# Kernel tuning notes

Hardware: AMD Instinct MI355X
Metric: run time of the kernel (lower is better)

The kernel has to match this reference:

```python
import jax, jax.numpy as jnp
import numpy as np

N_NODES = 4096
EDGE_PROB = 0.01


def setup_inputs() -> dict:
    key = jax.random.key(0)
    kx, ka, kw = jax.random.split(key, 3)
    x = jax.random.normal(kx, (4, 32, N_NODES, 12), dtype=jnp.float32)
    u = jax.random.uniform(ka, (N_NODES, N_NODES), dtype=jnp.float32)
    adj = (u < EDGE_PROB).astype(jnp.float32)
    adj = jnp.maximum(adj, adj.T)
    weight = jax.random.normal(kw, (3, 32, 32), dtype=jnp.float32) * 0.1
    bias = jnp.zeros((32,), dtype=jnp.float32)
    return {"x": x, "adj": adj, "weight": weight, "bias": bias}


def reference(x, adj, weight, bias):
    # x: [B, c_in, N, T] -> [B, T, N, c_in] as in AdaptiveGraphConv.forward
    B, C, N, T = x.shape
    h = jnp.transpose(x, (0, 3, 2, 1))  # [B, T, N, C]
    # DenseChebConv (K=3): L = I - D^{-1/2} A D^{-1/2}, inf -> 0 for isolated nodes
    d = adj.sum(axis=-1)
    d_inv_sqrt = jnp.where(d > 0, jnp.where(d > 0, d, 1.0) ** -0.5, 0.0)
    norm_adj = d_inv_sqrt[:, None] * adj * d_inv_sqrt[None, :]
    L = jnp.eye(N, dtype=x.dtype) - norm_adj
    Tx0 = h
    Tx1 = jnp.einsum('mn,btnc->btmc', L, h)
    Tx2 = 2.0 * jnp.einsum('mn,btnc->btmc', L, Tx1) - Tx0
    out = (jnp.einsum('btnc,co->btno', Tx0, weight[0])
           + jnp.einsum('btnc,co->btno', Tx1, weight[1])
           + jnp.einsum('btnc,co->btno', Tx2, weight[2])
           + bias)
    # back to [B, c_out, N, T]
    return jnp.transpose(out, (0, 3, 2, 1))
```

## Files before the change

### kernel.cpp

```cpp
#include <hip/hip_runtime.h>

#define NN 4096
#define CC 32
#define TT 12
#define BB 4
#define BT 48
#define NC 1536
#define MAXD 192
#define FW 512
#define NCH 3
#define STP 36
#define SOP 33

typedef float f32x4 __attribute__((ext_vector_type(4)));
typedef short short8 __attribute__((ext_vector_type(8)));
typedef unsigned short ushort8 __attribute__((ext_vector_type(8)));

__device__ __forceinline__ float bf2f(unsigned short h) {
  return __uint_as_float(((unsigned int)h) << 16);
}
__device__ __forceinline__ unsigned short f2bf(float f) {
  unsigned int u = __float_as_uint(f);
  return (unsigned short)((u + 0x7FFFu + ((u >> 16) & 1u)) >> 16);
}
__device__ __forceinline__ float blo(unsigned int w) { return __uint_as_float(w << 16); }
__device__ __forceinline__ float bhi(unsigned int w) { return __uint_as_float(w & 0xFFFF0000u); }

__global__ __launch_bounds__(256) void k_build_trans(const float* __restrict__ adj,
                                                     const float* __restrict__ x,
                                                     uint2* __restrict__ edges,
                                                     int* __restrict__ deg,
                                                     float* __restrict__ dis,
                                                     unsigned short* __restrict__ H) {
  __shared__ unsigned short sT[192 * STP];
  __shared__ unsigned short lcol[4][1024];
  __shared__ int wcnt[4];
  if (blockIdx.x < NN) {
    int m = blockIdx.x;
    int w = threadIdx.x >> 6, lane = threadIdx.x & 63;
    const float* row = adj + (size_t)m * NN + w * 1024;
    unsigned long long ltmask = (1ull << lane) - 1ull;
    int cnt = 0;
    #pragma unroll
    for (int it = 0; it < 16; ++it) {
      float f = row[it * 64 + lane];
      unsigned long long ball = __ballot(f != 0.0f);
      if (f != 0.0f)
        lcol[w][cnt + __popcll(ball & ltmask)] = (unsigned short)(w * 1024 + it * 64 + lane);
      cnt += __popcll(ball);
    }
    if (lane == 0) wcnt[w] = cnt;
    __syncthreads();
    int c0 = wcnt[0], c1 = wcnt[1], c2 = wcnt[2], c3 = wcnt[3];
    int base = (w == 0) ? 0 : (w == 1) ? c0 : (w == 2) ? c0 + c1 : c0 + c1 + c2;
    int total = c0 + c1 + c2 + c3;
    unsigned int* ecol = (unsigned int*)(edges + m * MAXD);
    for (int i = lane; i < cnt; i += 64) {
      int p = base + i;
      if (p < MAXD) ecol[p * 2] = (unsigned int)lcol[w][i];
    }
    if (threadIdx.x == 0) {
      int d = total < MAXD ? total : MAXD;
      deg[m] = d;
      dis[m] = d > 0 ? (float)(1.0 / sqrt((double)d)) : 0.0f;
    }
  } else {
    int bx = blockIdx.x - NN;
    int b = bx >> 8;
    int n0 = (bx & 255) * 16;
    int c = threadIdx.x >> 3;
    int l8 = threadIdx.x & 7;
    size_t base = ((size_t)(b * CC + c) * NN + n0) * TT;
    #pragma unroll
    for (int it = 0; it < 6; ++it) {
      int j0 = it * 32 + l8 * 4;
      float4 f = *(const float4*)(x + base + j0);
      sT[(j0 + 0) * STP + c] = f2bf(f.x);
      sT[(j0 + 1) * STP + c] = f2bf(f.y);
      sT[(j0 + 2) * STP + c] = f2bf(f.z);
      sT[(j0 + 3) * STP + c] = f2bf(f.w);
    }
    __syncthreads();
    #pragma unroll
    for (int k = 0; k < 6; ++k) {
      int p = (threadIdx.x >> 3) + 32 * k;
      int nl = p / TT, t = p - nl * TT;
      ushort4 v = *(const ushort4*)&sT[p * STP + l8 * 4];
      size_t off = ((size_t)(n0 + nl) * BT + b * TT + t) * CC + l8 * 4;
      *(ushort4*)(H + off) = v;
    }
  }
}

__global__ __launch_bounds__(192) void k_wt(uint2* __restrict__ edges,
                                            const int* __restrict__ deg,
                                            int* __restrict__ degp,
                                            const float* __restrict__ dis) {
  int m = blockIdx.x;
  int j = threadIdx.x;
  int d = deg[m];
  int dp = (d + 15) & ~15;
  if (j < d) {
    unsigned int* e = (unsigned int*)(edges + m * MAXD + j);
    e[1] = __float_as_uint(dis[e[0]]);
  } else if (j < dp) {
    edges[m * MAXD + j] = make_uint2((unsigned int)m, 0u);
  }
  if (j == 0) degp[m] = dp;
}

__global__ __launch_bounds__(1024) void k_gather(const unsigned short* __restrict__ S,
                                                 const uint2* __restrict__ edges,
                                                 const int* __restrict__ degp,
                                                 const float* __restrict__ dis,
                                                 unsigned short* __restrict__ D) {
  int tid = threadIdx.x;
  int wid = __builtin_amdgcn_readfirstlane(tid >> 6);
  int lane = tid & 63;
  int m = blockIdx.x * 16 + wid;
  int d = degp[m];
  float dm = dis[m];
  const uint2* ep = edges + (size_t)m * MAXD;
  const unsigned short* Sy = S + blockIdx.y * FW;
  int lo2 = lane * 8;
  float a0 = 0.f, a1 = 0.f, a2 = 0.f, a3 = 0.f;
  float a4 = 0.f, a5 = 0.f, a6 = 0.f, a7 = 0.f;
  for (int e = 0; e < d; e += 8) {
    uint4 hv[8];
    float w[8];
    #pragma unroll
    for (int k = 0; k < 8; ++k) {
      uint2 ew = ep[e + k];
      w[k] = __uint_as_float(ew.y);
      hv[k] = *(const uint4*)(Sy + (int)ew.x * NC + lo2);
    }
    #pragma unroll
    for (int k = 0; k < 8; ++k) {
      float wk = w[k];
      a0 = fmaf(wk, blo(hv[k].x), a0); a1 = fmaf(wk, bhi(hv[k].x), a1);
      a2 = fmaf(wk, blo(hv[k].y), a2); a3 = fmaf(wk, bhi(hv[k].y), a3);
      a4 = fmaf(wk, blo(hv[k].z), a4); a5 = fmaf(wk, bhi(hv[k].z), a5);
      a6 = fmaf(wk, blo(hv[k].w), a6); a7 = fmaf(wk, bhi(hv[k].w), a7);
    }
  }
  int fo = blockIdx.y * FW + lo2;
  ushort8 o;
  o[0] = f2bf(dm * a0); o[1] = f2bf(dm * a1);
  o[2] = f2bf(dm * a2); o[3] = f2bf(dm * a3);
  o[4] = f2bf(dm * a4); o[5] = f2bf(dm * a5);
  o[6] = f2bf(dm * a6); o[7] = f2bf(dm * a7);
  *(ushort8*)(D + (size_t)m * NC + fo) = o;
}

#define SEGST(bS, tS, lS, rr) {                                              \
    const int nq = (lS) / 4;                                                 \
    int o = (rr) / (16 * nq);                                                \
    int rem = (rr) - o * (16 * nq);                                          \
    int nl = rem / nq, q = rem - nl * nq;                                    \
    int rw = (bS) * 12 + (tS) + q * 4 - yy * 16;                             \
    float4 v = make_float4(sOut[nl][rw + 0][o], sOut[nl][rw + 1][o],         \
                           sOut[nl][rw + 2][o], sOut[nl][rw + 3][o]);        \
    size_t gb = (((size_t)((bS) * CC + o) * NN) + n0 + nl) * TT + (tS) + q * 4; \
    *(float4*)(out + gb) = v; }

__global__ __launch_bounds__(1024) void k_gmix(
    const unsigned short* __restrict__ G1,
    const unsigned short* __restrict__ H,
    const uint2* __restrict__ edges,
    const int* __restrict__ degp,
    const float* __restrict__ dis,
    const float* __restrict__ W,
    const float* __restrict__ bias,
    float* __restrict__ out) {
  __shared__ __align__(16) unsigned short sG2[16][16][CC];
  __shared__ __align__(16) float sOut[16][16][SOP];
  int tid = threadIdx.x;
  int wid = __builtin_amdgcn_readfirstlane(tid >> 6);
  int lane = tid & 63;
  int n0 = blockIdx.x * 16;
  int m = n0 + wid;
  int yy = blockIdx.y;
  int d = degp[m];
  float dm = dis[m];
  const uint2* ep = edges + (size_t)m * MAXD;
  const unsigned short* Sy = G1 + yy * FW;
  int lo2 = lane * 8;
  float a0 = 0.f, a1 = 0.f, a2 = 0.f, a3 = 0.f;
  float a4 = 0.f, a5 = 0.f, a6 = 0.f, a7 = 0.f;
  for (int e = 0; e < d; e += 8) {
    uint4 hv[8];
    float w[8];
    #pragma unroll
    for (int k = 0; k < 8; ++k) {
      uint2 ew = ep[e + k];
      w[k] = __uint_as_float(ew.y);
      hv[k] = *(const uint4*)(Sy + (int)ew.x * NC + lo2);
    }
    #pragma unroll
    for (int k = 0; k < 8; ++k) {
      float wk = w[k];
      a0 = fmaf(wk, blo(hv[k].x), a0); a1 = fmaf(wk, bhi(hv[k].x), a1);
      a2 = fmaf(wk, blo(hv[k].y), a2); a3 = fmaf(wk, bhi(hv[k].y), a3);
      a4 = fmaf(wk, blo(hv[k].z), a4); a5 = fmaf(wk, bhi(hv[k].z), a5);
      a6 = fmaf(wk, blo(hv[k].w), a6); a7 = fmaf(wk, bhi(hv[k].w), a7);
    }
  }
  ushort8 go;
  go[0] = f2bf(dm * a0); go[1] = f2bf(dm * a1);
  go[2] = f2bf(dm * a2); go[3] = f2bf(dm * a3);
  go[4] = f2bf(dm * a4); go[5] = f2bf(dm * a5);
  go[6] = f2bf(dm * a6); go[7] = f2bf(dm * a7);
  *(ushort8*)&sG2[wid][lane >> 2][(lane & 3) * 8] = go;
  int lm = lane & 15, quad = lane >> 4;
  size_t abase = ((size_t)m * BT + yy * 16 + lm) * CC + quad * 8;
  short8 af0 = *(const short8*)(H + abase);
  short8 af1 = *(const short8*)(G1 + abase);
  short8 af2 = *(const short8*)&sG2[wid][lm][quad * 8];
  #pragma unroll
  for (int h = 0; h < 2; ++h) {
    float bs = bias[h * 16 + lm];
    f32x4 acc = {bs, bs, bs, bs};
    #pragma unroll
    for (int g = 0; g < 3; ++g) {
      short8 vh, vl;
      #pragma unroll
      for (int j = 0; j < 8; ++j) {
        int r = quad * 8 + j, c = h * 16 + lm;
        float w0 = W[(0 * CC + r) * CC + c];
        float w1 = W[(1 * CC + r) * CC + c];
        float w2 = W[(2 * CC + r) * CC + c];
        float w = (g == 0) ? (w0 + w1 + w2)
                 : (g == 1) ? (-w1 - 4.f * w2)
                            : (2.f * w2);
        unsigned short hi = f2bf(w);
        vh[j] = (short)hi;
        vl[j] = (short)f2bf(w - bf2f(hi));
      }
      short8 af = (g == 0) ? af0 : (g == 1) ? af1 : af2;
      acc = __builtin_amdgcn_mfma_f32_16x16x32_bf16(af, vh, acc, 0, 0, 0);
      acc = __builtin_amdgcn_mfma_f32_16x16x32_bf16(af, vl, acc, 0, 0, 0);
    }
    int o = h * 16 + lm;
    #pragma unroll
    for (int reg = 0; reg < 4; ++reg)
      sOut[wid][quad * 4 + reg][o] = acc[reg];
  }
  __syncthreads();
  if (yy == 0) {
    #pragma unroll
    for (int j = 0; j < 2; ++j) {
      int idx = j * 1024 + tid;
      if (idx < 1536) SEGST(0, 0, 12, idx) else SEGST(1, 0, 4, idx - 1536)
    }
  } else if (yy == 1) {
    #pragma unroll
    for (int j = 0; j < 2; ++j) {
      int idx = j * 1024 + tid;
      if (idx < 1024) SEGST(1, 4, 8, idx) else SEGST(2, 0, 8, idx - 1024)
    }
  } else {
    #pragma unroll
    for (int j = 0; j < 2; ++j) {
      int idx = j * 1024 + tid;
      if (idx < 512) SEGST(2, 8, 4, idx) else SEGST(3, 0, 12, idx - 512)
    }
  }
}

extern "C" void kernel_launch(void* const* d_in, const int* in_sizes, int n_in,
                              void* d_out, int out_size, void* d_ws, size_t ws_size,
                              hipStream_t stream) {
  const float* x    = (const float*)d_in[0];
  const float* adj  = (const float*)d_in[1];
  const float* wgt  = (const float*)d_in[2];
  const float* bias = (const float*)d_in[3];
  char* ws = (char*)d_ws;
  float* dis  = (float*)ws;
  int*   deg  = (int*)(ws + 16384);
  int*   degp = (int*)(ws + 32768);
  uint2* edges = (uint2*)(ws + 49152);
  char* p = ws + 49152 + (size_t)NN * MAXD * 8;
  unsigned short* H  = (unsigned short*)p;
  unsigned short* G1 = (unsigned short*)(p + (size_t)NN * NC * 2);

  k_build_trans<<<NN + 1024, 256, 0, stream>>>(adj, x, edges, deg, dis, H);
  k_wt<<<NN, 192, 0, stream>>>(edges, deg, degp, dis);
  k_gather<<<dim3(NN / 16, NCH), 1024, 0, stream>>>(H, edges, degp, dis, G1);
  k_gmix<<<dim3(NN / 16, NCH), 1024, 0, stream>>>(G1, H, edges, degp, dis,
                                                  wgt, bias, (float*)d_out);
}
```

Measured before the change: 251.3 us.

## Split build and transpose kernels, use atomic shared counter for edge extraction

Splits the combined adjacency-scan and input-transpose kernel into separate k_build and k_trans launches. The adjacency scan switches from ordered per-wave ballot compaction to vectorized uint4 row loads with a shared atomic counter. This makes neighbor order nondeterministic, which can change float summation order. The sOut shared array also gains a padded dimension, and the extra launch adds some overhead.

```diff
diff --git a/kernel.cpp b/kernel.cpp
--- a/kernel.cpp
+++ b/kernel.cpp
@@ -26,69 +26,31 @@
 __device__ __forceinline__ float blo(unsigned int w) { return __uint_as_float(w << 16); }
 __device__ __forceinline__ float bhi(unsigned int w) { return __uint_as_float(w & 0xFFFF0000u); }
 
-__global__ __launch_bounds__(256) void k_build_trans(const float* __restrict__ adj,
-                                                     const float* __restrict__ x,
-                                                     uint2* __restrict__ edges,
-                                                     int* __restrict__ deg,
-                                                     float* __restrict__ dis,
-                                                     unsigned short* __restrict__ H) {
-  __shared__ unsigned short sT[192 * STP];
-  __shared__ unsigned short lcol[4][1024];
-  __shared__ int wcnt[4];
-  if (blockIdx.x < NN) {
-    int m = blockIdx.x;
-    int w = threadIdx.x >> 6, lane = threadIdx.x & 63;
-    const float* row = adj + (size_t)m * NN + w * 1024;
-    unsigned long long ltmask = (1ull << lane) - 1ull;
-    int cnt = 0;
-    #pragma unroll
-    for (int it = 0; it < 16; ++it) {
-      float f = row[it * 64 + lane];
-      unsigned long long ball = __ballot(f != 0.0f);
-      if (f != 0.0f)
-        lcol[w][cnt + __popcll(ball & ltmask)] = (unsigned short)(w * 1024 + it * 64 + lane);
-      cnt += __popcll(ball);
-    }
-    if (lane == 0) wcnt[w] = cnt;
-    __syncthreads();
-    int c0 = wcnt[0], c1 = wcnt[1], c2 = wcnt[2], c3 = wcnt[3];
-    int base = (w == 0) ? 0 : (w == 1) ? c0 : (w == 2) ? c0 + c1 : c0 + c1 + c2;
-    int total = c0 + c1 + c2 + c3;
-    unsigned int* ecol = (unsigned int*)(edges + m * MAXD);
-    for (int i = lane; i < cnt; i += 64) {
-      int p = base + i;
-      if (p < MAXD) ecol[p * 2] = (unsigned int)lcol[w][i];
-    }
-    if (threadIdx.x == 0) {
-      int d = total < MAXD ? total : MAXD;
-      deg[m] = d;
-      dis[m] = d > 0 ? (float)(1.0 / sqrt((double)d)) : 0.0f;
-    }
-  } else {
-    int bx = blockIdx.x - NN;
-    int b = bx >> 8;
-    int n0 = (bx & 255) * 16;
-    int c = threadIdx.x >> 3;
-    int l8 = threadIdx.x & 7;
-    size_t base = ((size_t)(b * CC + c) * NN + n0) * TT;
-    #pragma unroll
-    for (int it = 0; it < 6; ++it) {
-      int j0 = it * 32 + l8 * 4;
-      float4 f = *(const float4*)(x + base + j0);
-      sT[(j0 + 0) * STP + c] = f2bf(f.x);
-      sT[(j0 + 1) * STP + c] = f2bf(f.y);
-      sT[(j0 + 2) * STP + c] = f2bf(f.z);
-      sT[(j0 + 3) * STP + c] = f2bf(f.w);
-    }
-    __syncthreads();
-    #pragma unroll
-    for (int k = 0; k < 6; ++k) {
-      int p = (threadIdx.x >> 3) + 32 * k;
-      int nl = p / TT, t = p - nl * TT;
-      ushort4 v = *(const ushort4*)&sT[p * STP + l8 * 4];
-      size_t off = ((size_t)(n0 + nl) * BT + b * TT + t) * CC + l8 * 4;
-      *(ushort4*)(H + off) = v;
-    }
+__global__ __launch_bounds__(256) void k_build(const float* __restrict__ adj,
+                                               uint2* __restrict__ edges,
+                                               int* __restrict__ deg, float* __restrict__ dis) {
+  __shared__ int cnt;
+  int m = blockIdx.x;
+  if (threadIdx.x == 0) cnt = 0;
+  __syncthreads();
+  unsigned int* ecol = (unsigned int*)(edges + m * MAXD);
+  const uint4* row = (const uint4*)(adj + (size_t)m * NN);
+  for (int i = threadIdx.x; i < NN / 4; i += 256) {
+    uint4 v = row[i];
+    unsigned int ws[4] = {v.x, v.y, v.z, v.w};
+    #pragma unroll
+    for (int k = 0; k < 4; ++k) {
+      if (ws[k] != 0) {
+        int p = atomicAdd(&cnt, 1);
+        if (p < MAXD) ecol[p * 2] = (unsigned int)(i * 4 + k);
+      }
+    }
+  }
+  __syncthreads();
+  if (threadIdx.x == 0) {
+    int d = cnt < MAXD ? cnt : MAXD;
+    deg[m] = d;
+    dis[m] = d > 0 ? (float)(1.0 / sqrt((double)d)) : 0.0f;
   }
 }
 
@@ -107,6 +69,34 @@
     edges[m * MAXD + j] = make_uint2((unsigned int)m, 0u);
   }
   if (j == 0) degp[m] = dp;
+}
+
+__global__ __launch_bounds__(256) void k_trans(const float* __restrict__ x,
+                                               unsigned short* __restrict__ H) {
+  __shared__ unsigned short sT[192 * STP];
+  int b = blockIdx.x >> 8;
+  int n0 = (blockIdx.x & 255) * 16;
+  int c = threadIdx.x >> 3;
+  int l8 = threadIdx.x & 7;
+  size_t base = ((size_t)(b * CC + c) * NN + n0) * TT;
+  #pragma unroll
+  for (int it = 0; it < 6; ++it) {
+    int j0 = it * 32 + l8 * 4;
+    float4 f = *(const float4*)(x + base + j0);
+    sT[(j0 + 0) * STP + c] = f2bf(f.x);
+    sT[(j0 + 1) * STP + c] = f2bf(f.y);
+    sT[(j0 + 2) * STP + c] = f2bf(f.z);
+    sT[(j0 + 3) * STP + c] = f2bf(f.w);
+  }
+  __syncthreads();
+  #pragma unroll
+  for (int k = 0; k < 6; ++k) {
+    int p = (threadIdx.x >> 3) + 32 * k;
+    int nl = p / TT, t = p - nl * TT;
+    ushort4 v = *(const ushort4*)&sT[p * STP + l8 * 4];
+    size_t off = ((size_t)(n0 + nl) * BT + b * TT + t) * CC + l8 * 4;
+    *(ushort4*)(H + off) = v;
+  }
 }
 
 __global__ __launch_bounds__(1024) void k_gather(const unsigned short* __restrict__ S,
@@ -173,7 +163,7 @@
     const float* __restrict__ bias,
     float* __restrict__ out) {
   __shared__ __align__(16) unsigned short sG2[16][16][CC];
-  __shared__ __align__(16) float sOut[16][16][SOP];
+  __shared__ __align__(16) float sOut[16][17][SOP];
   int tid = threadIdx.x;
   int wid = __builtin_amdgcn_readfirstlane(tid >> 6);
   int lane = tid & 63;
@@ -283,8 +273,9 @@
   unsigned short* H  = (unsigned short*)p;
   unsigned short* G1 = (unsigned short*)(p + (size_t)NN * NC * 2);
 
-  k_build_trans<<<NN + 1024, 256, 0, stream>>>(adj, x, edges, deg, dis, H);
+  k_build<<<NN, 256, 0, stream>>>(adj, edges, deg, dis);
   k_wt<<<NN, 192, 0, stream>>>(edges, deg, degp, dis);
+  k_trans<<<1024, 256, 0, stream>>>(x, H);
   k_gather<<<dim3(NN / 16, NCH), 1024, 0, stream>>>(H, edges, degp, dis, G1);
   k_gmix<<<dim3(NN / 16, NCH), 1024, 0, stream>>>(G1, H, edges, degp, dis,
                                                   wgt, bias, (float*)d_out);
```

After: 238.2 us. 1.06x faster.
